# Kernel tuning notes

Measured on AMD Instinct MI355X. Metric: run time of the kernel, lower is better.

The kernel has to match this reference:

```python
import jax, jax.numpy as jnp
import numpy as np

B, T, C, HD = 4, 4096, 2048, 128  # batch, block_size, n_embadding, head_dim


def _precompute_cos_sin(dim, end, theta=10000.0):
    freqs = 1.0 / theta ** (np.arange(0, dim, 2)[: dim // 2].astype(np.float32) / dim)
    t = np.arange(end, dtype=np.float32)
    ang = np.outer(t, freqs)  # [T, HD/2]
    return jnp.asarray(np.cos(ang), jnp.float32), jnp.asarray(np.sin(ang), jnp.float32)


def setup_inputs() -> dict:
    key = jax.random.key(0)
    k0, k1, k2, k3 = jax.random.split(key, 4)
    scale = 1.0 / np.sqrt(C).astype(np.float32)
    x = jax.random.normal(k0, (B, T, C), jnp.float32)
    Wq = jax.random.normal(k1, (HD, C), jnp.float32) * scale
    Wk = jax.random.normal(k2, (HD, C), jnp.float32) * scale
    Wv = jax.random.normal(k3, (HD, C), jnp.float32) * scale
    cos, sin = _precompute_cos_sin(HD, T)
    return {"x": x, "Wq": Wq, "Wk": Wk, "Wv": Wv, "cos": cos, "sin": sin}


def _rope(v, cos, sin):
    # v: [B, T, HD]; complex multiply on (even, odd) pairs
    v2 = v.reshape(*v.shape[:-1], -1, 2)  # [B, T, HD/2, 2]
    vr, vi = v2[..., 0], v2[..., 1]
    c = cos[None, :, :]  # [1, T, HD/2]
    s = sin[None, :, :]
    out_r = vr * c - vi * s
    out_i = vr * s + vi * c
    return jnp.stack([out_r, out_i], axis=-1).reshape(v.shape)


def reference(x, Wq, Wk, Wv, cos, sin):
    Bx, Tx, Cx = x.shape
    q = jnp.einsum('btc,dc->btd', x, Wq)
    k = jnp.einsum('btc,dc->btd', x, Wk)
    q = _rope(q, cos, sin)
    k = _rope(k, cos, sin)
    # NOTE: original scales by full embedding dim C, not head_dim
    scores = jnp.einsum('btd,bsd->bts', q, k) * (Cx ** -0.5)
    causal = jnp.tril(jnp.ones((Tx, Tx), bool))
    scores = jnp.where(causal[None, :, :], scores, -jnp.inf)
    w = jax.nn.softmax(scores, axis=-1)
    v = jnp.einsum('btc,dc->btd', x, Wv)
    return jnp.einsum('bts,bsd->btd', w, v)
```

## Files before the change

kernel.cpp:

```cpp
#include <hip/hip_runtime.h>

#define B_ 4
#define T_ 4096
#define C_ 2048
#define HD_ 128
#define M_ (B_*T_)

typedef __bf16 bf8 __attribute__((ext_vector_type(8)));
typedef unsigned short u16x8 __attribute__((ext_vector_type(8)));
typedef unsigned short u16x4 __attribute__((ext_vector_type(4)));
typedef float f32x4 __attribute__((ext_vector_type(4)));

typedef __attribute__((address_space(3))) unsigned char lds_u8_t;
typedef __attribute__((address_space(1))) const unsigned char gm_u8_t;

__device__ __forceinline__ void glds16(const void* g, void* l) {
    __builtin_amdgcn_global_load_lds((gm_u8_t*)g, (lds_u8_t*)l, 16, 0, 0);
}

__device__ __forceinline__ unsigned short f2bf(float f) {
    unsigned u = __builtin_bit_cast(unsigned, f);
    u += 0x7FFFu + ((u >> 16) & 1u);
    return (unsigned short)(u >> 16);
}
__device__ __forceinline__ float bf2f(unsigned short h) {
    unsigned u = ((unsigned)h) << 16;
    return __builtin_bit_cast(float, u);
}
__device__ __forceinline__ bf8 ld_bf8(const unsigned short* p) {
    u16x8 t = *(const u16x8*)p;
    return __builtin_bit_cast(bf8, t);
}
__device__ __forceinline__ f32x4 zero4() { f32x4 v = {0.f,0.f,0.f,0.f}; return v; }

__global__ __launch_bounds__(256) void wconv(
    const float* __restrict__ Wq, const float* __restrict__ Wk,
    const float* __restrict__ Wv, unsigned short* __restrict__ wbf)
{
    int idx = blockIdx.x * 256 + threadIdx.x;
    int e = idx * 8;
    int z = e >> 18;
    int r = e & 262143;
    const float* src = (z == 0 ? Wq : z == 1 ? Wk : Wv) + r;
    float4 a = *(const float4*)src;
    float4 b = *(const float4*)(src + 4);
    u16x8 o;
    o[0]=f2bf(a.x); o[1]=f2bf(a.y); o[2]=f2bf(a.z); o[3]=f2bf(a.w);
    o[4]=f2bf(b.x); o[5]=f2bf(b.y); o[6]=f2bf(b.z); o[7]=f2bf(b.w);
    *(u16x8*)(wbf + e) = o;
}

__global__ __launch_bounds__(256) void qkv_gemm(
    const float* __restrict__ x, const unsigned short* __restrict__ wbf,
    const float* __restrict__ cosp, const float* __restrict__ sinp,
    unsigned short* __restrict__ qws, unsigned short* __restrict__ kws,
    unsigned short* __restrict__ vws)
{
    __shared__ __align__(16) float xs[64*64];
    __shared__ __align__(16) unsigned short ws2[128*64];

    const int tid = threadIdx.x;
    const int w = tid >> 6, l = tid & 63;
    const int g = blockIdx.x;
    const int xcd = g & 7;
    const int s = g >> 3;
    const int z = s % 3;
    const int mm = s / 3;
    const int mt = mm * 8 + xcd;
    const int rowbase = mt * 64;

    const int swz = l & 7;
    const int aq  = l >> 4;
    const int coll = l & 15;

    f32x4 acc[2][4];
    #pragma unroll
    for (int i = 0; i < 2; ++i)
        #pragma unroll
        for (int j = 0; j < 4; ++j) acc[i][j] = zero4();

    const unsigned short* wsrc = wbf + (size_t)z * (HD_ * C_);

    for (int kc = 0; kc < C_; kc += 64) {
        __syncthreads();
        #pragma unroll
        for (int c = 0; c < 4; ++c) {
            int row = w * 16 + c * 4 + aq;
            int fb = coll ^ (row & 7);
            glds16(x + (size_t)(rowbase + row) * C_ + kc + fb * 4,
                   (void*)&xs[(w * 16 + c * 4) * 64]);
        }
        #pragma unroll
        for (int c = 0; c < 4; ++c) {
            int row = w * 32 + c * 8 + (l >> 3);
            int fb = (l & 7) ^ (row & 7);
            glds16(wsrc + (size_t)row * C_ + kc + fb * 8,
                   (void*)&ws2[(w * 32 + c * 8) * 64]);
        }
        __syncthreads();

        #pragma unroll
        for (int ks_ = 0; ks_ < 2; ++ks_) {
            bf8 a[2];
            #pragma unroll
            for (int mi = 0; mi < 2; ++mi) {
                int row = (w & 1) * 32 + mi * 16 + coll;
                int s0 = ks_ * 8 + aq * 2;
                float4 fa = *(const float4*)&xs[row * 64 + ((s0 ^ swz) << 2)];
                float4 fb = *(const float4*)&xs[row * 64 + (((s0 + 1) ^ swz) << 2)];
                u16x8 t;
                t[0]=f2bf(fa.x); t[1]=f2bf(fa.y); t[2]=f2bf(fa.z); t[3]=f2bf(fa.w);
                t[4]=f2bf(fb.x); t[5]=f2bf(fb.y); t[6]=f2bf(fb.z); t[7]=f2bf(fb.w);
                a[mi] = __builtin_bit_cast(bf8, t);
            }
            #pragma unroll
            for (int nt = 0; nt < 4; ++nt) {
                int row = (w >> 1) * 64 + nt * 16 + coll;
                int slot = (ks_ * 4 + aq) ^ swz;
                bf8 bb = ld_bf8(&ws2[row * 64 + (slot << 3)]);
                acc[0][nt] = __builtin_amdgcn_mfma_f32_16x16x32_bf16(a[0], bb, acc[0][nt], 0, 0, 0);
                acc[1][nt] = __builtin_amdgcn_mfma_f32_16x16x32_bf16(a[1], bb, acc[1][nt], 0, 0, 0);
            }
        }
    }

    const int rl0 = aq * 4;
    const int cbase = (w >> 1) * 64;
    const int mrow = (w & 1) * 32;
    if (z < 2) {
        const float QSC = 0.022097086912079608f * 1.44269504088896340736f;
        const float fs = (z == 0) ? QSC : 1.0f;
        unsigned short* dst = (z == 0) ? qws : kws;
        #pragma unroll
        for (int mi = 0; mi < 2; ++mi) {
            #pragma unroll
            for (int nt = 0; nt < 4; ++nt) {
                int col = cbase + nt * 16 + coll;
                #pragma unroll
                for (int r = 0; r < 4; ++r) {
                    float val = acc[mi][nt][r];
                    float oth = __shfl_xor(val, 1, 64);
                    int grow = rowbase + mrow + mi * 16 + rl0 + r;
                    int t = grow & (T_ - 1);
                    if ((coll & 1) == 0) {
                        int i = col >> 1;
                        float cv = cosp[t * 64 + i], sv = sinp[t * 64 + i];
                        float o_r = (val * cv - oth * sv) * fs;
                        float o_i = (val * sv + oth * cv) * fs;
                        unsigned pack = (unsigned)f2bf(o_r) | ((unsigned)f2bf(o_i) << 16);
                        *(unsigned*)&dst[(size_t)grow * HD_ + col] = pack;
                    }
                }
            }
        }
    } else {
        const int bq = rowbase >> 12;
        #pragma unroll
        for (int mi = 0; mi < 2; ++mi) {
            int tb = (rowbase + mrow + mi * 16 + rl0) & (T_ - 1);
            #pragma unroll
            for (int nt = 0; nt < 4; ++nt) {
                int col = cbase + nt * 16 + coll;
                u16x4 pk;
                pk[0] = f2bf(acc[mi][nt][0]); pk[1] = f2bf(acc[mi][nt][1]);
                pk[2] = f2bf(acc[mi][nt][2]); pk[3] = f2bf(acc[mi][nt][3]);
                *(u16x4*)&vws[(size_t)(bq * HD_ + col) * T_ + tb] = pk;
            }
        }
    }
}

__global__ __launch_bounds__(256) void attn(
    const unsigned short* __restrict__ qws, const unsigned short* __restrict__ kws,
    const unsigned short* __restrict__ vws, float* __restrict__ out)
{
    __shared__ __align__(16) unsigned short qs[32*128];
    __shared__ __align__(16) unsigned short ks[64*128];
    __shared__ __align__(16) unsigned short vs[128*64];
    __shared__ __align__(16) unsigned short ps[32*72];
    __shared__ float lpart[4*16];

    const int tid = threadIdx.x;
    const int w = tid >> 6, l = tid & 63;
    int idx = blockIdx.x;
    int j = (idx < 256) ? idx : (767 - idx);
    const int b  = j & 3;
    const int qt = j >> 2;
    const int qbase = qt * 32;
    const size_t rowoff = (size_t)b * T_;

    const int swz = l & 7, aq = l >> 4, coll = l & 15;
    const int rh = (w & 1) * 16;
    const int cg = w >> 1;
    const int rl0 = aq * 4;

    #pragma unroll
    for (int c = 0; c < 2; ++c) {
        int row = w * 8 + c * 4 + aq;
        int fb = coll ^ (row & 7);
        glds16(qws + (rowoff + qbase + row) * HD_ + fb * 8,
               (void*)&qs[(w * 8 + c * 4) * 128]);
    }

    float l_r[4] = {0.f, 0.f, 0.f, 0.f};
    f32x4 accO[4];
    #pragma unroll
    for (int i = 0; i < 4; ++i) accO[i] = zero4();

    const int nst = (qt >> 1) + 1;

    for (int st = 0; st < nst; ++st) {
        const int sbase = st * 64;
        __syncthreads();
        #pragma unroll
        for (int c = 0; c < 4; ++c) {
            int row = w * 16 + c * 4 + aq;
            int fb = coll ^ (row & 7);
            glds16(kws + (rowoff + sbase + row) * HD_ + fb * 8,
                   (void*)&ks[(w * 16 + c * 4) * 128]);
        }
        #pragma unroll
        for (int c = 0; c < 4; ++c) {
            int row = w * 32 + c * 8 + (l >> 3);
            int fb = (l & 7) ^ (row & 7);
            glds16(vws + ((size_t)(b * HD_ + row)) * T_ + sbase + fb * 8,
                   (void*)&vs[(w * 32 + c * 8) * 64]);
        }
        __syncthreads();

        f32x4 sacc[2];
        sacc[0] = zero4(); sacc[1] = zero4();
        #pragma unroll
        for (int kk = 0; kk < 4; ++kk) {
            const int slot8 = ((kk * 4 + aq) ^ swz) << 3;
            bf8 a = ld_bf8(&qs[(rh + coll) * 128 + slot8]);
            #pragma unroll
            for (int nt = 0; nt < 2; ++nt) {
                bf8 bb = ld_bf8(&ks[(cg * 32 + nt * 16 + coll) * 128 + slot8]);
                sacc[nt] = __builtin_amdgcn_mfma_f32_16x16x32_bf16(a, bb, sacc[nt], 0, 0, 0);
            }
        }

        const bool masked = (st == nst - 1);
        #pragma unroll
        for (int r = 0; r < 4; ++r) {
            float s0 = sacc[0][r], s1 = sacc[1][r];
            if (masked) {
                int qi = qbase + rh + rl0 + r;
                int ki = sbase + cg * 32 + coll;
                s0 = (ki      > qi) ? -1e30f : s0;
                s1 = (ki + 16 > qi) ? -1e30f : s1;
            }
            float p0 = __builtin_amdgcn_exp2f(s0);
            float p1 = __builtin_amdgcn_exp2f(s1);
            unsigned short b0 = f2bf(p0), b1 = f2bf(p1);
            const int prow = (rh + rl0 + r) * 72;
            ps[prow + cg * 32 + coll]      = b0;
            ps[prow + cg * 32 + 16 + coll] = b1;
            l_r[r] += bf2f(b0) + bf2f(b1);
        }
        __syncthreads();

        #pragma unroll
        for (int kk = 0; kk < 2; ++kk) {
            bf8 a = ld_bf8(&ps[(rh + coll) * 72 + kk * 32 + aq * 8]);
            const int slot8 = ((kk * 4 + aq) ^ swz) << 3;
            #pragma unroll
            for (int nt = 0; nt < 4; ++nt) {
                bf8 bb = ld_bf8(&vs[(cg * 64 + nt * 16 + coll) * 64 + slot8]);
                accO[nt] = __builtin_amdgcn_mfma_f32_16x16x32_bf16(a, bb, accO[nt], 0, 0, 0);
            }
        }
    }

    #pragma unroll
    for (int r = 0; r < 4; ++r) {
        float s = l_r[r];
        s += __shfl_xor(s, 1, 64);
        s += __shfl_xor(s, 2, 64);
        s += __shfl_xor(s, 4, 64);
        s += __shfl_xor(s, 8, 64);
        l_r[r] = s;
    }
    if (coll == 0) {
        #pragma unroll
        for (int r = 0; r < 4; ++r) lpart[w * 16 + rl0 + r] = l_r[r];
    }
    __syncthreads();

    #pragma unroll
    for (int r = 0; r < 4; ++r) {
        float L = l_r[r] + lpart[(w ^ 2) * 16 + rl0 + r];
        float inv = 1.f / L;
        int grow = qbase + rh + rl0 + r;
        #pragma unroll
        for (int nt = 0; nt < 4; ++nt) {
            out[(rowoff + grow) * HD_ + cg * 64 + nt * 16 + coll] = accO[nt][r] * inv;
        }
    }
}

extern "C" void kernel_launch(void* const* d_in, const int* in_sizes, int n_in,
                              void* d_out, int out_size, void* d_ws, size_t ws_size,
                              hipStream_t stream) {
    const float* x    = (const float*)d_in[0];
    const float* Wq   = (const float*)d_in[1];
    const float* Wk   = (const float*)d_in[2];
    const float* Wv   = (const float*)d_in[3];
    const float* cosp = (const float*)d_in[4];
    const float* sinp = (const float*)d_in[5];
    float* out = (float*)d_out;

    unsigned short* qws = (unsigned short*)d_ws;
    unsigned short* kws = qws + (size_t)M_ * HD_;
    unsigned short* vws = kws + (size_t)M_ * HD_;
    unsigned short* wbf = vws + (size_t)M_ * HD_;

    wconv<<<dim3(384), dim3(256), 0, stream>>>(Wq, Wk, Wv, wbf);
    qkv_gemm<<<dim3(768), dim3(256), 0, stream>>>(x, wbf, cosp, sinp, qws, kws, vws);
    attn<<<dim3(B_ * (T_ / 32)), dim3(256), 0, stream>>>(qws, kws, vws, out);
}
```

Measured before the change: 309.6 us.

## Halve row tiles in QKV GEMM and attention to double grid size

The QKV projection now uses 32-row tiles instead of 64, and attention uses 16-query tiles instead of 32. Both launch twice as many blocks, with the attention wave split reworked so each wave owns 16 keys and 32 output columns. Manual bf16 rounding is also replaced with native __bf16 conversions. The aim is more parallelism and occupancy, at the cost of each block re-reading the weight and K/V tiles over fewer rows, which roughly doubles global traffic for W, K and V.

```diff
diff --git a/kernel.cpp b/kernel.cpp
--- a/kernel.cpp
+++ b/kernel.cpp
@@ -7,6 +7,8 @@
 #define M_ (B_*T_)
 
 typedef __bf16 bf8 __attribute__((ext_vector_type(8)));
+typedef __bf16 bf16x2 __attribute__((ext_vector_type(2)));
+typedef __bf16 bf16x4 __attribute__((ext_vector_type(4)));
 typedef unsigned short u16x8 __attribute__((ext_vector_type(8)));
 typedef unsigned short u16x4 __attribute__((ext_vector_type(4)));
 typedef float f32x4 __attribute__((ext_vector_type(4)));
@@ -18,14 +20,19 @@
     __builtin_amdgcn_global_load_lds((gm_u8_t*)g, (lds_u8_t*)l, 16, 0, 0);
 }
 
-__device__ __forceinline__ unsigned short f2bf(float f) {
-    unsigned u = __builtin_bit_cast(unsigned, f);
-    u += 0x7FFFu + ((u >> 16) & 1u);
-    return (unsigned short)(u >> 16);
-}
-__device__ __forceinline__ float bf2f(unsigned short h) {
-    unsigned u = ((unsigned)h) << 16;
-    return __builtin_bit_cast(float, u);
+__device__ __forceinline__ bf8 cvt_bf8(float4 a, float4 b) {
+    bf8 t;
+    t[0]=(__bf16)a.x; t[1]=(__bf16)a.y; t[2]=(__bf16)a.z; t[3]=(__bf16)a.w;
+    t[4]=(__bf16)b.x; t[5]=(__bf16)b.y; t[6]=(__bf16)b.z; t[7]=(__bf16)b.w;
+    return t;
+}
+__device__ __forceinline__ unsigned pk2(float a, float b) {
+    bf16x2 t; t[0] = (__bf16)a; t[1] = (__bf16)b;
+    return __builtin_bit_cast(unsigned, t);
+}
+__device__ __forceinline__ u16x4 pk4(float a, float b, float c, float d) {
+    bf16x4 t; t[0]=(__bf16)a; t[1]=(__bf16)b; t[2]=(__bf16)c; t[3]=(__bf16)d;
+    return __builtin_bit_cast(u16x4, t);
 }
 __device__ __forceinline__ bf8 ld_bf8(const unsigned short* p) {
     u16x8 t = *(const u16x8*)p;
@@ -44,10 +51,8 @@
     const float* src = (z == 0 ? Wq : z == 1 ? Wk : Wv) + r;
     float4 a = *(const float4*)src;
     float4 b = *(const float4*)(src + 4);
-    u16x8 o;
-    o[0]=f2bf(a.x); o[1]=f2bf(a.y); o[2]=f2bf(a.z); o[3]=f2bf(a.w);
-    o[4]=f2bf(b.x); o[5]=f2bf(b.y); o[6]=f2bf(b.z); o[7]=f2bf(b.w);
-    *(u16x8*)(wbf + e) = o;
+    bf8 o = cvt_bf8(a, b);
+    *(u16x8*)(wbf + e) = __builtin_bit_cast(u16x8, o);
 }
 
 __global__ __launch_bounds__(256) void qkv_gemm(
@@ -56,7 +61,7 @@
     unsigned short* __restrict__ qws, unsigned short* __restrict__ kws,
     unsigned short* __restrict__ vws)
 {
-    __shared__ __align__(16) float xs[64*64];
+    __shared__ __align__(16) float xs[32*64];
     __shared__ __align__(16) unsigned short ws2[128*64];
 
     const int tid = threadIdx.x;
@@ -67,28 +72,26 @@
     const int z = s % 3;
     const int mm = s / 3;
     const int mt = mm * 8 + xcd;
-    const int rowbase = mt * 64;
+    const int rowbase = mt * 32;
 
     const int swz = l & 7;
     const int aq  = l >> 4;
     const int coll = l & 15;
 
-    f32x4 acc[2][4];
+    f32x4 acc[4];
     #pragma unroll
-    for (int i = 0; i < 2; ++i)
-        #pragma unroll
-        for (int j = 0; j < 4; ++j) acc[i][j] = zero4();
+    for (int j = 0; j < 4; ++j) acc[j] = zero4();
 
     const unsigned short* wsrc = wbf + (size_t)z * (HD_ * C_);
 
     for (int kc = 0; kc < C_; kc += 64) {
         __syncthreads();
         #pragma unroll
-        for (int c = 0; c < 4; ++c) {
-            int row = w * 16 + c * 4 + aq;
+        for (int c = 0; c < 2; ++c) {
+            int row = w * 8 + c * 4 + aq;
             int fb = coll ^ (row & 7);
             glds16(x + (size_t)(rowbase + row) * C_ + kc + fb * 4,
-                   (void*)&xs[(w * 16 + c * 4) * 64]);
+                   (void*)&xs[(w * 8 + c * 4) * 64]);
         }
         #pragma unroll
         for (int c = 0; c < 4; ++c) {
@@ -101,71 +104,54 @@
 
         #pragma unroll
         for (int ks_ = 0; ks_ < 2; ++ks_) {
-            bf8 a[2];
-            #pragma unroll
-            for (int mi = 0; mi < 2; ++mi) {
-                int row = (w & 1) * 32 + mi * 16 + coll;
-                int s0 = ks_ * 8 + aq * 2;
-                float4 fa = *(const float4*)&xs[row * 64 + ((s0 ^ swz) << 2)];
-                float4 fb = *(const float4*)&xs[row * 64 + (((s0 + 1) ^ swz) << 2)];
-                u16x8 t;
-                t[0]=f2bf(fa.x); t[1]=f2bf(fa.y); t[2]=f2bf(fa.z); t[3]=f2bf(fa.w);
-                t[4]=f2bf(fb.x); t[5]=f2bf(fb.y); t[6]=f2bf(fb.z); t[7]=f2bf(fb.w);
-                a[mi] = __builtin_bit_cast(bf8, t);
-            }
+            int row = (w & 1) * 16 + coll;
+            int s0 = ks_ * 8 + aq * 2;
+            float4 fa = *(const float4*)&xs[row * 64 + ((s0 ^ swz) << 2)];
+            float4 fb = *(const float4*)&xs[row * 64 + (((s0 + 1) ^ swz) << 2)];
+            bf8 a = cvt_bf8(fa, fb);
             #pragma unroll
             for (int nt = 0; nt < 4; ++nt) {
-                int row = (w >> 1) * 64 + nt * 16 + coll;
+                int brow = (w >> 1) * 64 + nt * 16 + coll;
                 int slot = (ks_ * 4 + aq) ^ swz;
-                bf8 bb = ld_bf8(&ws2[row * 64 + (slot << 3)]);
-                acc[0][nt] = __builtin_amdgcn_mfma_f32_16x16x32_bf16(a[0], bb, acc[0][nt], 0, 0, 0);
-                acc[1][nt] = __builtin_amdgcn_mfma_f32_16x16x32_bf16(a[1], bb, acc[1][nt], 0, 0, 0);
+                bf8 bb = ld_bf8(&ws2[brow * 64 + (slot << 3)]);
+                acc[nt] = __builtin_amdgcn_mfma_f32_16x16x32_bf16(a, bb, acc[nt], 0, 0, 0);
             }
         }
     }
 
     const int rl0 = aq * 4;
     const int cbase = (w >> 1) * 64;
-    const int mrow = (w & 1) * 32;
+    const int mrow = (w & 1) * 16;
     if (z < 2) {
         const float QSC = 0.022097086912079608f * 1.44269504088896340736f;
         const float fs = (z == 0) ? QSC : 1.0f;
         unsigned short* dst = (z == 0) ? qws : kws;
         #pragma unroll
-        for (int mi = 0; mi < 2; ++mi) {
+        for (int nt = 0; nt < 4; ++nt) {
+            int col = cbase + nt * 16 + coll;
             #pragma unroll
-            for (int nt = 0; nt < 4; ++nt) {
-                int col = cbase + nt * 16 + coll;
-                #pragma unroll
-                for (int r = 0; r < 4; ++r) {
-                    float val = acc[mi][nt][r];
-                    float oth = __shfl_xor(val, 1, 64);
-                    int grow = rowbase + mrow + mi * 16 + rl0 + r;
-                    int t = grow & (T_ - 1);
-                    if ((coll & 1) == 0) {
-                        int i = col >> 1;
-                        float cv = cosp[t * 64 + i], sv = sinp[t * 64 + i];
-                        float o_r = (val * cv - oth * sv) * fs;
-                        float o_i = (val * sv + oth * cv) * fs;
-                        unsigned pack = (unsigned)f2bf(o_r) | ((unsigned)f2bf(o_i) << 16);
-                        *(unsigned*)&dst[(size_t)grow * HD_ + col] = pack;
-                    }
+            for (int r = 0; r < 4; ++r) {
+                float val = acc[nt][r];
+                float oth = __shfl_xor(val, 1, 64);
+                int grow = rowbase + mrow + rl0 + r;
+                int t = grow & (T_ - 1);
+                if ((coll & 1) == 0) {
+                    int i = col >> 1;
+                    float cv = cosp[t * 64 + i], sv = sinp[t * 64 + i];
+                    float o_r = (val * cv - oth * sv) * fs;
+                    float o_i = (val * sv + oth * cv) * fs;
+                    *(unsigned*)&dst[(size_t)grow * HD_ + col] = pk2(o_r, o_i);
                 }
             }
         }
     } else {
         const int bq = rowbase >> 12;
-        #pragma unroll
-        for (int mi = 0; mi < 2; ++mi) {
-            int tb = (rowbase + mrow + mi * 16 + rl0) & (T_ - 1);
-            #pragma unroll
-            for (int nt = 0; nt < 4; ++nt) {
-                int col = cbase + nt * 16 + coll;
-                u16x4 pk;
-                pk[0] = f2bf(acc[mi][nt][0]); pk[1] = f2bf(acc[mi][nt][1]);
-                pk[2] = f2bf(acc[mi][nt][2]); pk[3] = f2bf(acc[mi][nt][3]);
-                *(u16x4*)&vws[(size_t)(bq * HD_ + col) * T_ + tb] = pk;
-            }
+        int tb = (rowbase + mrow + rl0) & (T_ - 1);
+        #pragma unroll
+        for (int nt = 0; nt < 4; ++nt) {
+            int col = cbase + nt * 16 + coll;
+            u16x4 pk = pk4(acc[nt][0], acc[nt][1], acc[nt][2], acc[nt][3]);
+            *(u16x4*)&vws[(size_t)(bq * HD_ + col) * T_ + tb] = pk;
         }
     }
 }
@@ -174,40 +160,36 @@
     const unsigned short* __restrict__ qws, const unsigned short* __restrict__ kws,
     const unsigned short* __restrict__ vws, float* __restrict__ out)
 {
-    __shared__ __align__(16) unsigned short qs[32*128];
+    __shared__ __align__(16) unsigned short qs[16*128];
     __shared__ __align__(16) unsigned short ks[64*128];
     __shared__ __align__(16) unsigned short vs[128*64];
-    __shared__ __align__(16) unsigned short ps[32*72];
+    __shared__ __align__(16) unsigned short ps[16*72];
     __shared__ float lpart[4*16];
 
     const int tid = threadIdx.x;
     const int w = tid >> 6, l = tid & 63;
     int idx = blockIdx.x;
-    int j = (idx < 256) ? idx : (767 - idx);
+    int j = (idx < 512) ? idx : (1535 - idx);
     const int b  = j & 3;
     const int qt = j >> 2;
-    const int qbase = qt * 32;
+    const int qbase = qt * 16;
     const size_t rowoff = (size_t)b * T_;
 
     const int swz = l & 7, aq = l >> 4, coll = l & 15;
-    const int rh = (w & 1) * 16;
-    const int cg = w >> 1;
     const int rl0 = aq * 4;
 
-    #pragma unroll
-    for (int c = 0; c < 2; ++c) {
-        int row = w * 8 + c * 4 + aq;
+    {
+        int row = w * 4 + aq;
         int fb = coll ^ (row & 7);
         glds16(qws + (rowoff + qbase + row) * HD_ + fb * 8,
-               (void*)&qs[(w * 8 + c * 4) * 128]);
+               (void*)&qs[(w * 4) * 128]);
     }
 
     float l_r[4] = {0.f, 0.f, 0.f, 0.f};
-    f32x4 accO[4];
-    #pragma unroll
-    for (int i = 0; i < 4; ++i) accO[i] = zero4();
-
-    const int nst = (qt >> 1) + 1;
+    f32x4 accO[2];
+    accO[0] = zero4(); accO[1] = zero4();
+
+    const int nst = (qt >> 2) + 1;
 
     for (int st = 0; st < nst; ++st) {
         const int sbase = st * 64;
@@ -228,46 +210,38 @@
         }
         __syncthreads();
 
-        f32x4 sacc[2];
-        sacc[0] = zero4(); sacc[1] = zero4();
+        f32x4 sacc = zero4();
         #pragma unroll
         for (int kk = 0; kk < 4; ++kk) {
             const int slot8 = ((kk * 4 + aq) ^ swz) << 3;
-            bf8 a = ld_bf8(&qs[(rh + coll) * 128 + slot8]);
+            bf8 a = ld_bf8(&qs[coll * 128 + slot8]);
+            bf8 bb = ld_bf8(&ks[(w * 16 + coll) * 128 + slot8]);
+            sacc = __builtin_amdgcn_mfma_f32_16x16x32_bf16(a, bb, sacc, 0, 0, 0);
+        }
+
+        const bool masked = (st == nst - 1);
+        #pragma unroll
+        for (int r = 0; r < 4; ++r) {
+            float sv = sacc[r];
+            if (masked) {
+                int qi = qbase + rl0 + r;
+                int ki = sbase + w * 16 + coll;
+                sv = (ki > qi) ? -1e30f : sv;
+            }
+            float p = __builtin_amdgcn_exp2f(sv);
+            __bf16 pb = (__bf16)p;
+            ps[(rl0 + r) * 72 + w * 16 + coll] = __builtin_bit_cast(unsigned short, pb);
+            l_r[r] += (float)pb;
+        }
+        __syncthreads();
+
+        #pragma unroll
+        for (int kk = 0; kk < 2; ++kk) {
+            bf8 a = ld_bf8(&ps[coll * 72 + kk * 32 + aq * 8]);
+            const int slot8 = ((kk * 4 + aq) ^ swz) << 3;
             #pragma unroll
             for (int nt = 0; nt < 2; ++nt) {
-                bf8 bb = ld_bf8(&ks[(cg * 32 + nt * 16 + coll) * 128 + slot8]);
-                sacc[nt] = __builtin_amdgcn_mfma_f32_16x16x32_bf16(a, bb, sacc[nt], 0, 0, 0);
-            }
-        }
-
-        const bool masked = (st == nst - 1);
-        #pragma unroll
-        for (int r = 0; r < 4; ++r) {
-            float s0 = sacc[0][r], s1 = sacc[1][r];
-            if (masked) {
-                int qi = qbase + rh + rl0 + r;
-                int ki = sbase + cg * 32 + coll;
-                s0 = (ki      > qi) ? -1e30f : s0;
-                s1 = (ki + 16 > qi) ? -1e30f : s1;
-            }
-            float p0 = __builtin_amdgcn_exp2f(s0);
-            float p1 = __builtin_amdgcn_exp2f(s1);
-            unsigned short b0 = f2bf(p0), b1 = f2bf(p1);
-            const int prow = (rh + rl0 + r) * 72;
-            ps[prow + cg * 32 + coll]      = b0;
-            ps[prow + cg * 32 + 16 + coll] = b1;
-            l_r[r] += bf2f(b0) + bf2f(b1);
-        }
-        __syncthreads();
-
-        #pragma unroll
-        for (int kk = 0; kk < 2; ++kk) {
-            bf8 a = ld_bf8(&ps[(rh + coll) * 72 + kk * 32 + aq * 8]);
-            const int slot8 = ((kk * 4 + aq) ^ swz) << 3;
-            #pragma unroll
-            for (int nt = 0; nt < 4; ++nt) {
-                bf8 bb = ld_bf8(&vs[(cg * 64 + nt * 16 + coll) * 64 + slot8]);
+                bf8 bb = ld_bf8(&vs[(w * 32 + nt * 16 + coll) * 64 + slot8]);
                 accO[nt] = __builtin_amdgcn_mfma_f32_16x16x32_bf16(a, bb, accO[nt], 0, 0, 0);
             }
         }
@@ -290,12 +264,13 @@
 
     #pragma unroll
     for (int r = 0; r < 4; ++r) {
-        float L = l_r[r] + lpart[(w ^ 2) * 16 + rl0 + r];
+        float L = (lpart[0 * 16 + rl0 + r] + lpart[1 * 16 + rl0 + r])
+                + (lpart[2 * 16 + rl0 + r] + lpart[3 * 16 + rl0 + r]);
         float inv = 1.f / L;
-        int grow = qbase + rh + rl0 + r;
-        #pragma unroll
-        for (int nt = 0; nt < 4; ++nt) {
-            out[(rowoff + grow) * HD_ + cg * 64 + nt * 16 + coll] = accO[nt][r] * inv;
+        int grow = qbase + rl0 + r;
+        #pragma unroll
+        for (int nt = 0; nt < 2; ++nt) {
+            out[(rowoff + grow) * HD_ + w * 32 + nt * 16 + coll] = accO[nt][r] * inv;
         }
     }
 }
@@ -317,6 +292,6 @@
     unsigned short* wbf = vws + (size_t)M_ * HD_;
 
     wconv<<<dim3(384), dim3(256), 0, stream>>>(Wq, Wk, Wv, wbf);
-    qkv_gemm<<<dim3(768), dim3(256), 0, stream>>>(x, wbf, cosp, sinp, qws, kws, vws);
-    attn<<<dim3(B_ * (T_ / 32)), dim3(256), 0, stream>>>(qws, kws, vws, out);
-}
+    qkv_gemm<<<dim3(1536), dim3(256), 0, stream>>>(x, wbf, cosp, sinp, qws, kws, vws);
+    attn<<<dim3(B_ * (T_ / 16)), dim3(256), 0, stream>>>(qws, kws, vws, out);
+}
```

Measured after the change: 326.3 us. 5.4% more time.
